# Performance work log

Measured on AMD Instinct MI355X. Metric: run time of the kernel, lower is better.

The kernel has to match this reference:

```python
import jax, jax.numpy as jnp
import numpy as np

L, H, V, T, E = 12, 12, 50257, 1024, 768
DH = E // H
EPS = 1e-5


def _ln(x, g, b):
    mu = jnp.mean(x, axis=-1, keepdims=True)
    var = jnp.mean(jnp.square(x - mu), axis=-1, keepdims=True)
    return g * (x - mu) * jax.lax.rsqrt(var + EPS) + b


def _gelu(x):
    # tanh-approx gelu as in the source
    return 0.5 * x * (1.0 + jnp.tanh(jnp.sqrt(2.0 / jnp.pi) * (x + 0.044715 * jnp.power(x, 3))))


def setup_inputs() -> dict:
    key = jax.random.key(0)
    ks = jax.random.split(key, 12)
    s = 0.02
    return {
        "x": jax.random.randint(ks[0], (8, T), 0, V),
        "tok_emb": jax.random.normal(ks[1], (V, E), jnp.float32) * s,
        "pos_emb": jax.random.normal(ks[2], (T, E), jnp.float32) * s,
        "ln1_g": jnp.ones((L, E), jnp.float32),
        "ln1_b": jnp.zeros((L, E), jnp.float32),
        "Wqkv": jax.random.normal(ks[3], (L, E, 3 * E), jnp.float32) * s,
        "bqkv": jnp.zeros((L, 3 * E), jnp.float32),
        "Wo": jax.random.normal(ks[4], (L, E, E), jnp.float32) * s,
        "bo": jnp.zeros((L, E), jnp.float32),
        "ln2_g": jnp.ones((L, E), jnp.float32),
        "ln2_b": jnp.zeros((L, E), jnp.float32),
        "W1": jax.random.normal(ks[5], (L, E, 4 * E), jnp.float32) * s,
        "b1": jnp.zeros((L, 4 * E), jnp.float32),
        "W2": jax.random.normal(ks[6], (L, 4 * E, E), jnp.float32) * s,
        "b2": jnp.zeros((L, E), jnp.float32),
        "lnf_g": jnp.ones((E,), jnp.float32),
        "lnf_b": jnp.zeros((E,), jnp.float32),
    }


def _gpt2(x, tok_emb, pos_emb, ln1_g, ln1_b, Wqkv, bqkv, Wo, bo,
          ln2_g, ln2_b, W1, b1, W2, b2, lnf_g, lnf_b):
    B, S = x.shape
    h = tok_emb[x] + pos_emb[:S][None, :, :]  # [B,S,E]
    mask = (jnp.arange(S)[:, None] >= jnp.arange(S)[None, :]).astype(jnp.float32)  # [S,S]
    mask = mask[None, None]  # [1,1,S,S]
    scale = jax.lax.rsqrt(jnp.float32(DH))
    for l in range(L):
        a = _ln(h, ln1_g[l], ln1_b[l])
        qkv = jnp.einsum('bse,ef->bsf', a, Wqkv[l]) + bqkv[l]
        q, k, v = jnp.split(qkv, 3, axis=-1)
        q = q.reshape(B, S, H, DH).transpose(0, 2, 1, 3)
        k = k.reshape(B, S, H, DH).transpose(0, 2, 1, 3)
        v = v.reshape(B, S, H, DH).transpose(0, 2, 1, 3)
        w = jnp.einsum('bhqd,bhkd->bhqk', q, k) * scale
        w = w * mask - 1e10 * (1.0 - mask)
        w = jax.nn.softmax(w, axis=-1)
        ctx = jnp.einsum('bhqk,bhkd->bhqd', w, v)
        ctx = ctx.transpose(0, 2, 1, 3).reshape(B, S, E)
        h = h + jnp.einsum('bse,ef->bsf', ctx, Wo[l]) + bo[l]
        a2 = _ln(h, ln2_g[l], ln2_b[l])
        ff = _gelu(jnp.einsum('bse,ef->bsf', a2, W1[l]) + b1[l])
        h = h + jnp.einsum('bsf,fe->bse', ff, W2[l]) + b2[l]
    h = _ln(h, lnf_g, lnf_b)
    last = h[:, -1, :]  # [B,E]
    return jnp.matmul(last, tok_emb.T)  # [B,V]


def reference(x, tok_emb, pos_emb, ln1_g, ln1_b, Wqkv, bqkv, Wo, bo,
              ln2_g, ln2_b, W1, b1, W2, b2, lnf_g, lnf_b):
    return _gpt2(x, tok_emb, pos_emb, ln1_g, ln1_b, Wqkv, bqkv, Wo, bo,
                 ln2_g, ln2_b, W1, b1, W2, b2, lnf_g, lnf_b)
```

## Files before the change

### kernel.cpp

```cpp
#include <hip/hip_runtime.h>
#include <math.h>

#define LNUM 12
#define HNUM 12
#define EMB 768
#define TSEQ 1024
#define BBATCH 8
#define VOCAB 50257
#define NTOK (BBATCH*TSEQ)

typedef unsigned short u16;
typedef __bf16 bf16_8 __attribute__((ext_vector_type(8)));
typedef float f32x4 __attribute__((ext_vector_type(4)));

__device__ __forceinline__ u16 f2bf(float f){
  unsigned u = __float_as_uint(f);
  u += 0x7fffu + ((u >> 16) & 1u);
  return (u16)(u >> 16);
}
__device__ __forceinline__ float wred(float v){
  #pragma unroll
  for (int m = 32; m; m >>= 1) v += __shfl_xor(v, m, 64);
  return v;
}

#define GLOAD_LDS16(g, l) \
  __builtin_amdgcn_global_load_lds((const __attribute__((address_space(1))) void*)(g), \
                                   (__attribute__((address_space(3))) void*)(l), 16, 0, 0)

__global__ __launch_bounds__(256) void tcvt_kernel(const float* __restrict__ src,
                                                   u16* __restrict__ dst, int K, int N){
  __shared__ float tile[32][33];
  size_t off = (size_t)blockIdx.z * K * N;
  const float* s = src + off;
  u16* d = dst + off;
  int n0 = blockIdx.x * 32, k0 = blockIdx.y * 32;
  int tx = threadIdx.x & 31, ty = threadIdx.x >> 5;
  #pragma unroll
  for (int i = 0; i < 4; i++)
    tile[ty + i*8][tx] = s[(size_t)(k0 + ty + i*8) * N + n0 + tx];
  __syncthreads();
  #pragma unroll
  for (int i = 0; i < 4; i++){
    int n = ty + i*8;
    d[(size_t)(n0 + n) * K + k0 + tx] = f2bf(tile[tx][n]);
  }
}

__global__ __launch_bounds__(256) void embed_kernel(const int* __restrict__ x,
    const float* __restrict__ tok, const float* __restrict__ pos, float* __restrict__ h){
  int row = blockIdx.x;
  int t = row & (TSEQ - 1);
  int id = x[row];
  const float* te = tok + (size_t)id * EMB;
  const float* pe = pos + (size_t)t * EMB;
  float* hr = h + (size_t)row * EMB;
  for (int i = threadIdx.x; i < EMB; i += 256) hr[i] = te[i] + pe[i];
}

template<int OBF, int LAST>
__global__ __launch_bounds__(256) void ln_kernel(const float* __restrict__ x,
    const float* __restrict__ g, const float* __restrict__ b, void* __restrict__ out){
  int orow, row;
  if (LAST){ orow = blockIdx.x; row = blockIdx.x * TSEQ + (TSEQ - 1); }
  else     { orow = row = blockIdx.x; }
  const float* xr = x + (size_t)row * EMB;
  int tid = threadIdx.x;
  int wave = tid >> 6, lane = tid & 63;
  float v[3];
  float s = 0.f;
  #pragma unroll
  for (int i = 0; i < 3; i++){ v[i] = xr[tid + i*256]; s += v[i]; }
  __shared__ float red[4];
  s = wred(s);
  if (lane == 0) red[wave] = s;
  __syncthreads();
  float mu = (red[0] + red[1] + red[2] + red[3]) * (1.f / EMB);
  float ss = 0.f;
  #pragma unroll
  for (int i = 0; i < 3; i++){ float d = v[i] - mu; ss += d * d; }
  __syncthreads();
  ss = wred(ss);
  if (lane == 0) red[wave] = ss;
  __syncthreads();
  float var = (red[0] + red[1] + red[2] + red[3]) * (1.f / EMB);
  float rs = rsqrtf(var + 1e-5f);
  #pragma unroll
  for (int i = 0; i < 3; i++){
    int e = tid + i*256;
    float o = g[e] * (v[i] - mu) * rs + b[e];
    if (OBF) ((u16*)out)[(size_t)orow * EMB + e] = f2bf(o);
    else     ((float*)out)[(size_t)orow * EMB + e] = o;
  }
}

template<int EPI>
__global__ __launch_bounds__(256) void gemm_bt(const u16* __restrict__ A,
    const u16* __restrict__ Bt, const float* __restrict__ bias,
    const float* __restrict__ resid, void* __restrict__ outp, int K, int N){
  __shared__ __align__(16) u16 lA[128*32];
  __shared__ __align__(16) u16 lB[128*32];
  const int tid = threadIdx.x;
  const int wave = tid >> 6, lane = tid & 63;
  const int bm = blockIdx.y, bn = blockIdx.x;
  const int wm = wave >> 1, wn = wave & 1;

  const u16* ga = A  + (size_t)(bm*128 + wave*32 + (lane >> 2)) * K + (lane & 3) * 8;
  const u16* gb = Bt + (size_t)(bn*128 + wave*32 + (lane >> 2)) * K + (lane & 3) * 8;
  u16* la = lA + wave * 32 * 32;
  u16* lb = lB + wave * 32 * 32;

  f32x4 acc[4][4];
  #pragma unroll
  for (int i = 0; i < 4; i++)
    #pragma unroll
    for (int j = 0; j < 4; j++){ f32x4 z = {0.f,0.f,0.f,0.f}; acc[i][j] = z; }

  const bf16_8* pa = (const bf16_8*)(lA + ((wm*64) + (lane & 15)) * 32 + (lane >> 4) * 8);
  const bf16_8* pb = (const bf16_8*)(lB + ((wn*64) + (lane & 15)) * 32 + (lane >> 4) * 8);

  for (int k0 = 0; k0 < K; k0 += 32){
    GLOAD_LDS16(ga,                 la);
    GLOAD_LDS16(ga + (size_t)16*K,  la + 16*32);
    GLOAD_LDS16(gb,                 lb);
    GLOAD_LDS16(gb + (size_t)16*K,  lb + 16*32);
    ga += 32; gb += 32;
    __syncthreads();
    bf16_8 af[4], bfv[4];
    #pragma unroll
    for (int i = 0; i < 4; i++){ af[i] = pa[i*64]; bfv[i] = pb[i*64]; }
    #pragma unroll
    for (int mi = 0; mi < 4; mi++)
      #pragma unroll
      for (int ni = 0; ni < 4; ni++)
        acc[mi][ni] = __builtin_amdgcn_mfma_f32_16x16x32_bf16(af[mi], bfv[ni], acc[mi][ni], 0, 0, 0);
    __syncthreads();
  }

  const int colb = bn*128 + wn*64;
  const int rowb = bm*128 + wm*64;
  #pragma unroll
  for (int ni = 0; ni < 4; ni++){
    int col = colb + ni*16 + (lane & 15);
    float bv = bias[col];
    #pragma unroll
    for (int mi = 0; mi < 4; mi++){
      #pragma unroll
      for (int j = 0; j < 4; j++){
        int row = rowb + mi*16 + (lane >> 4) * 4 + j;
        float v = acc[mi][ni][j] + bv;
        if (EPI == 1) v += resid[(size_t)row * N + col];
        if (EPI == 2){
          float y = 0.7978845608028654f * (v + 0.044715f * v * v * v);
          float e = __expf(fminf(2.f * y, 80.f));
          v = v * e / (e + 1.f);
        }
        if (EPI == 3 && col < 768) v *= 0.125f;
        if (EPI == 2 || EPI == 3) ((u16*)outp)[(size_t)row * N + col] = f2bf(v);
        else                      ((float*)outp)[(size_t)row * N + col] = v;
      }
    }
  }
}

__global__ __launch_bounds__(256) void vtrans_kernel(const u16* __restrict__ qkvb,
                                                     u16* __restrict__ vt){
  int wave = threadIdx.x >> 6, lane = threadIdx.x & 63;
  int bh = blockIdx.y, b = bh / HNUM, h = bh - b * HNUM;
  int t0 = blockIdx.x * 16 + wave * 4;
  const u16* src = qkvb + (size_t)b * TSEQ * 2304 + 1536 + h * 64 + lane;
  unsigned long long w = 0;
  #pragma unroll
  for (int i = 0; i < 4; i++)
    w |= (unsigned long long)src[(size_t)(t0 + i) * 2304] << (16 * i);
  *(unsigned long long*)(vt + ((size_t)bh * 64 + lane) * TSEQ + t0) = w;
}

__global__ __launch_bounds__(256) void attn_mfma(const u16* __restrict__ qkvb,
                                                 const u16* __restrict__ vt,
                                                 u16* __restrict__ ctx){
  __shared__ u16 plds[4][32][40];
  const int wave = threadIdx.x >> 6, lane = threadIdx.x & 63;
  const int g = lane >> 4, q15 = lane & 15;
  const int bh = blockIdx.y, b = bh / HNUM, h = bh - b * HNUM;
  const int q0 = blockIdx.x * 128 + wave * 32;
  const u16* qk  = qkvb + (size_t)b * TSEQ * 2304 + h * 64;
  const u16* vtb = vt + (size_t)bh * 64 * TSEQ;

  bf16_8 qfr[2][2];
  #pragma unroll
  for (int qf = 0; qf < 2; qf++)
    #pragma unroll
    for (int kc = 0; kc < 2; kc++)
      qfr[qf][kc] = *(const bf16_8*)(qk + (size_t)(q0 + qf*16 + q15) * 2304 + kc*32 + g*8);

  f32x4 oacc[2][4];
  #pragma unroll
  for (int i = 0; i < 2; i++)
    #pragma unroll
    for (int j = 0; j < 4; j++){ f32x4 z = {0.f,0.f,0.f,0.f}; oacc[i][j] = z; }
  float mx[2] = {-1e30f, -1e30f}, lsum[2] = {0.f, 0.f};

  for (int kb = 0; kb <= q0; kb += 32){
    bf16_8 kfr[2][2];
    #pragma unroll
    for (int kf = 0; kf < 2; kf++)
      #pragma unroll
      for (int kc = 0; kc < 2; kc++)
        kfr[kf][kc] = *(const bf16_8*)(qk + (size_t)(kb + kf*16 + q15) * 2304 + 768 + kc*32 + g*8);

    f32x4 s[2][2];
    #pragma unroll
    for (int kf = 0; kf < 2; kf++)
      #pragma unroll
      for (int qf = 0; qf < 2; qf++){
        f32x4 z = {0.f,0.f,0.f,0.f};
        #pragma unroll
        for (int kc = 0; kc < 2; kc++)
          z = __builtin_amdgcn_mfma_f32_16x16x32_bf16(kfr[kf][kc], qfr[qf][kc], z, 0, 0, 0);
        s[kf][qf] = z;
      }

    if (kb == q0){
      #pragma unroll
      for (int kf = 0; kf < 2; kf++)
        #pragma unroll
        for (int qf = 0; qf < 2; qf++)
          #pragma unroll
          for (int j = 0; j < 4; j++)
            if (kf*16 + g*4 + j > qf*16 + q15) s[kf][qf][j] = -1e30f;
    }

    bf16_8 vb[4];
    #pragma unroll
    for (int dc = 0; dc < 4; dc++)
      vb[dc] = *(const bf16_8*)(vtb + (size_t)(dc*16 + q15) * TSEQ + kb + g*8);

    #pragma unroll
    for (int qf = 0; qf < 2; qf++){
      float sm = -1e30f;
      #pragma unroll
      for (int kf = 0; kf < 2; kf++)
        #pragma unroll
        for (int j = 0; j < 4; j++) sm = fmaxf(sm, s[kf][qf][j]);
      sm = fmaxf(sm, __shfl_xor(sm, 16, 64));
      sm = fmaxf(sm, __shfl_xor(sm, 32, 64));
      float mn = fmaxf(mx[qf], sm);
      float c = __expf(mx[qf] - mn);
      mx[qf] = mn;
      float ps = 0.f;
      unsigned long long pw[2];
      #pragma unroll
      for (int kf = 0; kf < 2; kf++){
        unsigned long long w = 0;
        #pragma unroll
        for (int j = 0; j < 4; j++){
          float p = __expf(s[kf][qf][j] - mn);
          ps += p;
          w |= (unsigned long long)f2bf(p) << (16 * j);
        }
        pw[kf] = w;
      }
      ps += __shfl_xor(ps, 16, 64);
      ps += __shfl_xor(ps, 32, 64);
      lsum[qf] = lsum[qf] * c + ps;
      *(unsigned long long*)&plds[wave][qf*16 + q15][g*4]      = pw[0];
      *(unsigned long long*)&plds[wave][qf*16 + q15][16 + g*4] = pw[1];
      #pragma unroll
      for (int j = 0; j < 4; j++){
        float cr = __shfl(c, g*4 + j, 64);
        #pragma unroll
        for (int dc = 0; dc < 4; dc++) oacc[qf][dc][j] *= cr;
      }
    }

    asm volatile("s_waitcnt lgkmcnt(0)" ::: "memory");
    __builtin_amdgcn_sched_barrier(0);

    bf16_8 pa[2];
    pa[0] = *(const bf16_8*)&plds[wave][q15][g*8];
    pa[1] = *(const bf16_8*)&plds[wave][16 + q15][g*8];
    #pragma unroll
    for (int qf = 0; qf < 2; qf++)
      #pragma unroll
      for (int dc = 0; dc < 4; dc++)
        oacc[qf][dc] = __builtin_amdgcn_mfma_f32_16x16x32_bf16(pa[qf], vb[dc], oacc[qf][dc], 0, 0, 0);
  }

  u16* cb = ctx + ((size_t)(b * TSEQ + q0)) * EMB + h * 64;
  #pragma unroll
  for (int qf = 0; qf < 2; qf++){
    float inv = 1.f / lsum[qf];
    #pragma unroll
    for (int j = 0; j < 4; j++){
      float ir = __shfl(inv, g*4 + j, 64);
      int row = qf*16 + g*4 + j;
      #pragma unroll
      for (int dc = 0; dc < 4; dc++)
        cb[(size_t)row * EMB + dc*16 + q15] = f2bf(oacc[qf][dc][j] * ir);
    }
  }
}

__global__ __launch_bounds__(256) void logits_kernel(const float* __restrict__ last,
    const float* __restrict__ tok, float* __restrict__ out){
  __shared__ float ls[BBATCH * EMB];
  for (int i = threadIdx.x; i < BBATCH * EMB; i += 256) ls[i] = last[i];
  __syncthreads();
  int wave = threadIdx.x >> 6, lane = threadIdx.x & 63;
  int v = blockIdx.x * 4 + wave;
  if (v >= VOCAB) return;
  const float* tp = tok + (size_t)v * EMB;
  float acc[BBATCH];
  #pragma unroll
  for (int b = 0; b < BBATCH; b++) acc[b] = 0.f;
  #pragma unroll
  for (int i = 0; i < EMB/64; i++){
    float tv = tp[i*64 + lane];
    #pragma unroll
    for (int b = 0; b < BBATCH; b++) acc[b] += tv * ls[b*EMB + i*64 + lane];
  }
  #pragma unroll
  for (int b = 0; b < BBATCH; b++){
    float r = wred(acc[b]);
    if (lane == 0) out[(size_t)b * VOCAB + v] = r;
  }
}

extern "C" void kernel_launch(void* const* d_in, const int* in_sizes, int n_in,
                              void* d_out, int out_size, void* d_ws, size_t ws_size,
                              hipStream_t stream){
  const int*   x    = (const int*)  d_in[0];
  const float* tok  = (const float*)d_in[1];
  const float* pos  = (const float*)d_in[2];
  const float* ln1g = (const float*)d_in[3];
  const float* ln1b = (const float*)d_in[4];
  const float* Wqkv = (const float*)d_in[5];
  const float* bqkv = (const float*)d_in[6];
  const float* Wo   = (const float*)d_in[7];
  const float* bo   = (const float*)d_in[8];
  const float* ln2g = (const float*)d_in[9];
  const float* ln2b = (const float*)d_in[10];
  const float* W1   = (const float*)d_in[11];
  const float* b1   = (const float*)d_in[12];
  const float* W2   = (const float*)d_in[13];
  const float* b2   = (const float*)d_in[14];
  const float* lnfg = (const float*)d_in[15];
  const float* lnfb = (const float*)d_in[16];

  char* p = (char*)d_ws;
  u16* wqkvT = (u16*)p;  p += (size_t)LNUM*2304*768*2;
  u16* woT   = (u16*)p;  p += (size_t)LNUM*768*768*2;
  u16* w1T   = (u16*)p;  p += (size_t)LNUM*3072*768*2;
  u16* w2T   = (u16*)p;  p += (size_t)LNUM*768*3072*2;
  float* h   = (float*)p; p += (size_t)NTOK*EMB*4;
  u16* abuf  = (u16*)p;  p += (size_t)NTOK*EMB*2;
  void* tmp  = (void*)p; p += (size_t)NTOK*2304*4;
  u16* vt    = (u16*)p;  p += (size_t)BBATCH*HNUM*64*TSEQ*2;
  float* lastb = (float*)p; p += (size_t)BBATCH*EMB*4;
  if (ws_size < (size_t)(p - (char*)d_ws)) return;

  tcvt_kernel<<<dim3(2304/32, 768/32, LNUM), 256, 0, stream>>>(Wqkv, wqkvT, 768, 2304);
  tcvt_kernel<<<dim3(768/32,  768/32, LNUM), 256, 0, stream>>>(Wo,   woT,   768, 768);
  tcvt_kernel<<<dim3(3072/32, 768/32, LNUM), 256, 0, stream>>>(W1,   w1T,   768, 3072);
  tcvt_kernel<<<dim3(768/32, 3072/32, LNUM), 256, 0, stream>>>(W2,   w2T,   3072, 768);
  embed_kernel<<<NTOK, 256, 0, stream>>>(x, tok, pos, h);

  u16* qkvb = (u16*)tmp;
  u16* ff   = (u16*)tmp;
  for (int l = 0; l < LNUM; l++){
    ln_kernel<1,0><<<NTOK, 256, 0, stream>>>(h, ln1g + l*EMB, ln1b + l*EMB, abuf);
    gemm_bt<3><<<dim3(2304/128, NTOK/128), 256, 0, stream>>>(
        abuf, wqkvT + (size_t)l*2304*768, bqkv + (size_t)l*2304, nullptr, qkvb, 768, 2304);
    vtrans_kernel<<<dim3(TSEQ/16, BBATCH*HNUM), 256, 0, stream>>>(qkvb, vt);
    attn_mfma<<<dim3(TSEQ/128, BBATCH*HNUM), 256, 0, stream>>>(qkvb, vt, abuf);
    gemm_bt<1><<<dim3(768/128, NTOK/128), 256, 0, stream>>>(
        abuf, woT + (size_t)l*768*768, bo + (size_t)l*768, h, h, 768, 768);
    ln_kernel<1,0><<<NTOK, 256, 0, stream>>>(h, ln2g + l*EMB, ln2b + l*EMB, abuf);
    gemm_bt<2><<<dim3(3072/128, NTOK/128), 256, 0, stream>>>(
        abuf, w1T + (size_t)l*3072*768, b1 + (size_t)l*3072, nullptr, ff, 768, 3072);
    gemm_bt<1><<<dim3(768/128, NTOK/128), 256, 0, stream>>>(
        ff, w2T + (size_t)l*768*3072, b2 + (size_t)l*768, h, h, 3072, 768);
  }
  ln_kernel<0,1><<<BBATCH, 256, 0, stream>>>(h, lnfg, lnfb, lastb);
  logits_kernel<<<(VOCAB + 3)/4, 256, 0, stream>>>(lastb, tok, (float*)d_out);
}
```

Baseline: 4.333 ms.

## Pipeline GEMMs with 4-slot LDS ring and enlarge attention query tiles

Replaces the single-buffered 128x128 GEMM with a 512-thread kernel using larger tiles (128 or 256 by 256) and a four-slot LDS ring. Global-to-LDS loads are issued three K-steps ahead, and there is one barrier per step. This is meant to hide memory latency and cut synchronisation. Attention now gives each wave 64 query rows, prefetches the next K/V block into registers, and schedules the longest causal blocks first to improve load balance. The cost is higher register and LDS pressure, which may limit occupancy.

```diff
diff --git a/kernel.cpp b/kernel.cpp
--- a/kernel.cpp
+++ b/kernel.cpp
@@ -27,6 +27,8 @@
 #define GLOAD_LDS16(g, l) \
   __builtin_amdgcn_global_load_lds((const __attribute__((address_space(1))) void*)(g), \
                                    (__attribute__((address_space(3))) void*)(l), 16, 0, 0)
+
+template<int N> struct WCst { static constexpr int val = N; };
 
 __global__ __launch_bounds__(256) void tcvt_kernel(const float* __restrict__ src,
                                                    u16* __restrict__ dst, int K, int N){
@@ -94,60 +96,92 @@
   }
 }
 
-template<int EPI>
-__global__ __launch_bounds__(256) void gemm_bt(const u16* __restrict__ A,
+template<int BM, int EPI>
+__global__ __launch_bounds__(512, 2) void gemm_ring(const u16* __restrict__ A,
     const u16* __restrict__ Bt, const float* __restrict__ bias,
     const float* __restrict__ resid, void* __restrict__ outp, int K, int N){
-  __shared__ __align__(16) u16 lA[128*32];
-  __shared__ __align__(16) u16 lB[128*32];
+  constexpr int LA = BM / 128;
+  constexpr int LOADS = LA + 2;
+  constexpr int SLOTE = (BM + 256) * 32;
+  constexpr int M_REP = BM / 32;
+  __shared__ __align__(16) u16 lds[4 * SLOTE];
   const int tid = threadIdx.x;
   const int wave = tid >> 6, lane = tid & 63;
+  const int q15 = lane & 15, ko = lane >> 4;
+  const int wm = wave >> 2, wn = wave & 3;
   const int bm = blockIdx.y, bn = blockIdx.x;
-  const int wm = wave >> 1, wn = wave & 1;
-
-  const u16* ga = A  + (size_t)(bm*128 + wave*32 + (lane >> 2)) * K + (lane & 3) * 8;
-  const u16* gb = Bt + (size_t)(bn*128 + wave*32 + (lane >> 2)) * K + (lane & 3) * 8;
-  u16* la = lA + wave * 32 * 32;
-  u16* lb = lB + wave * 32 * 32;
-
-  f32x4 acc[4][4];
-  #pragma unroll
-  for (int i = 0; i < 4; i++)
+  const int NT = K >> 5;
+
+  const u16* gA0 = A  + (size_t)(bm*BM  + (tid >> 2)) * K + (tid & 3) * 8;
+  const u16* gB0 = Bt + (size_t)(bn*256 + (tid >> 2)) * K + (tid & 3) * 8;
+  u16* ldsW = lds + (tid >> 6) * 512;
+
+#define STAGE(tt) do { \
+    int _t = (tt); \
+    const u16* _sa = gA0 + (size_t)_t * 32; \
+    const u16* _sb = gB0 + (size_t)_t * 32; \
+    u16* _ls = ldsW + (_t & 3) * SLOTE; \
+    _Pragma("unroll") \
+    for (int _i = 0; _i < LA; _i++) \
+      GLOAD_LDS16(_sa + (size_t)_i * 128 * K, _ls + _i * 4096); \
+    _Pragma("unroll") \
+    for (int _i = 0; _i < 2; _i++) \
+      GLOAD_LDS16(_sb + (size_t)_i * 128 * K, _ls + BM*32 + _i * 4096); \
+  } while (0)
+
+  f32x4 acc[M_REP][4];
+  #pragma unroll
+  for (int i = 0; i < M_REP; i++)
     #pragma unroll
     for (int j = 0; j < 4; j++){ f32x4 z = {0.f,0.f,0.f,0.f}; acc[i][j] = z; }
 
-  const bf16_8* pa = (const bf16_8*)(lA + ((wm*64) + (lane & 15)) * 32 + (lane >> 4) * 8);
-  const bf16_8* pb = (const bf16_8*)(lB + ((wn*64) + (lane & 15)) * 32 + (lane >> 4) * 8);
-
-  for (int k0 = 0; k0 < K; k0 += 32){
-    GLOAD_LDS16(ga,                 la);
-    GLOAD_LDS16(ga + (size_t)16*K,  la + 16*32);
-    GLOAD_LDS16(gb,                 lb);
-    GLOAD_LDS16(gb + (size_t)16*K,  lb + 16*32);
-    ga += 32; gb += 32;
-    __syncthreads();
-    bf16_8 af[4], bfv[4];
-    #pragma unroll
-    for (int i = 0; i < 4; i++){ af[i] = pa[i*64]; bfv[i] = pb[i*64]; }
-    #pragma unroll
-    for (int mi = 0; mi < 4; mi++)
+  const int aoff = (wm*(BM/2) + q15) * 32 + ko * 8;
+  const int boff = BM*32 + (wn*64 + q15) * 32 + ko * 8;
+
+  auto tile = [&](int t, auto wc, bool dostage){
+    if (dostage) STAGE(t + 3);
+    const u16* sA = lds + (t & 3) * SLOTE;
+    bf16_8 af[M_REP], bfr[4];
+    #pragma unroll
+    for (int mi = 0; mi < M_REP; mi++) af[mi] = *(const bf16_8*)(sA + aoff + mi * 512);
+    #pragma unroll
+    for (int ni = 0; ni < 4; ni++)    bfr[ni] = *(const bf16_8*)(sA + boff + ni * 512);
+    __builtin_amdgcn_s_setprio(1);
+    #pragma unroll
+    for (int mi = 0; mi < M_REP; mi++)
       #pragma unroll
       for (int ni = 0; ni < 4; ni++)
-        acc[mi][ni] = __builtin_amdgcn_mfma_f32_16x16x32_bf16(af[mi], bfv[ni], acc[mi][ni], 0, 0, 0);
-    __syncthreads();
-  }
-
-  const int colb = bn*128 + wn*64;
-  const int rowb = bm*128 + wm*64;
+        acc[mi][ni] = __builtin_amdgcn_mfma_f32_16x16x32_bf16(af[mi], bfr[ni], acc[mi][ni], 0, 0, 0);
+    __builtin_amdgcn_s_setprio(0);
+    asm volatile("s_waitcnt vmcnt(%0)" :: "n"(decltype(wc)::val) : "memory");
+    __builtin_amdgcn_sched_barrier(0);
+    __builtin_amdgcn_s_barrier();
+    __builtin_amdgcn_sched_barrier(0);
+  };
+
+  STAGE(0); STAGE(1); STAGE(2);
+  asm volatile("s_waitcnt vmcnt(%0)" :: "n"(2 * LOADS) : "memory");
+  __builtin_amdgcn_sched_barrier(0);
+  __builtin_amdgcn_s_barrier();
+  __builtin_amdgcn_sched_barrier(0);
+
+  for (int t = 0; t < NT - 3; ++t) tile(t, WCst<2 * LOADS>{}, true);
+  tile(NT - 3, WCst<LOADS>{}, false);
+  tile(NT - 2, WCst<0>{}, false);
+  tile(NT - 1, WCst<0>{}, false);
+#undef STAGE
+
+  const int colb = bn*256 + wn*64;
+  const int rowb = bm*BM + wm*(BM/2);
   #pragma unroll
   for (int ni = 0; ni < 4; ni++){
-    int col = colb + ni*16 + (lane & 15);
+    int col = colb + ni*16 + q15;
     float bv = bias[col];
     #pragma unroll
-    for (int mi = 0; mi < 4; mi++){
+    for (int mi = 0; mi < M_REP; mi++){
       #pragma unroll
       for (int j = 0; j < 4; j++){
-        int row = rowb + mi*16 + (lane >> 4) * 4 + j;
+        int row = rowb + mi*16 + ko*4 + j;
         float v = acc[mi][ni][j] + bv;
         if (EPI == 1) v += resid[(size_t)row * N + col];
         if (EPI == 2){
@@ -176,68 +210,73 @@
   *(unsigned long long*)(vt + ((size_t)bh * 64 + lane) * TSEQ + t0) = w;
 }
 
-__global__ __launch_bounds__(256) void attn_mfma(const u16* __restrict__ qkvb,
-                                                 const u16* __restrict__ vt,
-                                                 u16* __restrict__ ctx){
-  __shared__ u16 plds[4][32][40];
+__global__ __launch_bounds__(256, 2) void attn_mfma(const u16* __restrict__ qkvb,
+                                                    const u16* __restrict__ vt,
+                                                    u16* __restrict__ ctx){
+  __shared__ u16 plds[4][64][40];
   const int wave = threadIdx.x >> 6, lane = threadIdx.x & 63;
   const int g = lane >> 4, q15 = lane & 15;
   const int bh = blockIdx.y, b = bh / HNUM, h = bh - b * HNUM;
-  const int q0 = blockIdx.x * 128 + wave * 32;
+  const int q0 = ((int)gridDim.x - 1 - (int)blockIdx.x) * 256 + wave * 64;
   const u16* qk  = qkvb + (size_t)b * TSEQ * 2304 + h * 64;
   const u16* vtb = vt + (size_t)bh * 64 * TSEQ;
 
-  bf16_8 qfr[2][2];
-  #pragma unroll
-  for (int qf = 0; qf < 2; qf++)
+#define LOADKV(kb_, kd, vd) do { \
+    _Pragma("unroll") \
+    for (int _kf = 0; _kf < 2; _kf++) \
+      _Pragma("unroll") \
+      for (int _kc = 0; _kc < 2; _kc++) \
+        kd[_kf][_kc] = *(const bf16_8*)(qk + (size_t)((kb_) + _kf*16 + q15) * 2304 + 768 + _kc*32 + g*8); \
+    _Pragma("unroll") \
+    for (int _dc = 0; _dc < 4; _dc++) \
+      vd[_dc] = *(const bf16_8*)(vtb + (size_t)(_dc*16 + q15) * TSEQ + (kb_) + g*8); \
+  } while (0)
+
+  bf16_8 qfr[4][2];
+  #pragma unroll
+  for (int qf = 0; qf < 4; qf++)
     #pragma unroll
     for (int kc = 0; kc < 2; kc++)
       qfr[qf][kc] = *(const bf16_8*)(qk + (size_t)(q0 + qf*16 + q15) * 2304 + kc*32 + g*8);
 
-  f32x4 oacc[2][4];
-  #pragma unroll
-  for (int i = 0; i < 2; i++)
+  f32x4 oacc[4][4];
+  #pragma unroll
+  for (int i = 0; i < 4; i++)
     #pragma unroll
     for (int j = 0; j < 4; j++){ f32x4 z = {0.f,0.f,0.f,0.f}; oacc[i][j] = z; }
-  float mx[2] = {-1e30f, -1e30f}, lsum[2] = {0.f, 0.f};
-
-  for (int kb = 0; kb <= q0; kb += 32){
-    bf16_8 kfr[2][2];
+  float mx[4] = {-1e30f,-1e30f,-1e30f,-1e30f}, lsum[4] = {0.f,0.f,0.f,0.f};
+
+  const int kbmax = q0 + 32;
+  bf16_8 kcur[2][2], vcur[4];
+  LOADKV(0, kcur, vcur);
+
+  for (int kb = 0; kb <= kbmax; kb += 32){
+    bf16_8 knxt[2][2], vnxt[4];
+    if (kb < kbmax) LOADKV(kb + 32, knxt, vnxt);
+
+    f32x4 s[2][4];
     #pragma unroll
     for (int kf = 0; kf < 2; kf++)
       #pragma unroll
-      for (int kc = 0; kc < 2; kc++)
-        kfr[kf][kc] = *(const bf16_8*)(qk + (size_t)(kb + kf*16 + q15) * 2304 + 768 + kc*32 + g*8);
-
-    f32x4 s[2][2];
-    #pragma unroll
-    for (int kf = 0; kf < 2; kf++)
-      #pragma unroll
-      for (int qf = 0; qf < 2; qf++){
+      for (int qf = 0; qf < 4; qf++){
         f32x4 z = {0.f,0.f,0.f,0.f};
-        #pragma unroll
-        for (int kc = 0; kc < 2; kc++)
-          z = __builtin_amdgcn_mfma_f32_16x16x32_bf16(kfr[kf][kc], qfr[qf][kc], z, 0, 0, 0);
+        z = __builtin_amdgcn_mfma_f32_16x16x32_bf16(kcur[kf][0], qfr[qf][0], z, 0, 0, 0);
+        z = __builtin_amdgcn_mfma_f32_16x16x32_bf16(kcur[kf][1], qfr[qf][1], z, 0, 0, 0);
         s[kf][qf] = z;
       }
 
-    if (kb == q0){
+    if (kb + 31 > q0){
       #pragma unroll
       for (int kf = 0; kf < 2; kf++)
         #pragma unroll
-        for (int qf = 0; qf < 2; qf++)
+        for (int qf = 0; qf < 4; qf++)
           #pragma unroll
           for (int j = 0; j < 4; j++)
-            if (kf*16 + g*4 + j > qf*16 + q15) s[kf][qf][j] = -1e30f;
+            if (kb + kf*16 + g*4 + j > q0 + qf*16 + q15) s[kf][qf][j] = -1e30f;
     }
 
-    bf16_8 vb[4];
-    #pragma unroll
-    for (int dc = 0; dc < 4; dc++)
-      vb[dc] = *(const bf16_8*)(vtb + (size_t)(dc*16 + q15) * TSEQ + kb + g*8);
-
-    #pragma unroll
-    for (int qf = 0; qf < 2; qf++){
+    #pragma unroll
+    for (int qf = 0; qf < 4; qf++){
       float sm = -1e30f;
       #pragma unroll
       for (int kf = 0; kf < 2; kf++)
@@ -277,19 +316,30 @@
     asm volatile("s_waitcnt lgkmcnt(0)" ::: "memory");
     __builtin_amdgcn_sched_barrier(0);
 
-    bf16_8 pa[2];
-    pa[0] = *(const bf16_8*)&plds[wave][q15][g*8];
-    pa[1] = *(const bf16_8*)&plds[wave][16 + q15][g*8];
-    #pragma unroll
-    for (int qf = 0; qf < 2; qf++)
+    bf16_8 pa[4];
+    #pragma unroll
+    for (int qf = 0; qf < 4; qf++)
+      pa[qf] = *(const bf16_8*)&plds[wave][qf*16 + q15][g*8];
+    #pragma unroll
+    for (int qf = 0; qf < 4; qf++)
       #pragma unroll
       for (int dc = 0; dc < 4; dc++)
-        oacc[qf][dc] = __builtin_amdgcn_mfma_f32_16x16x32_bf16(pa[qf], vb[dc], oacc[qf][dc], 0, 0, 0);
-  }
+        oacc[qf][dc] = __builtin_amdgcn_mfma_f32_16x16x32_bf16(pa[qf], vcur[dc], oacc[qf][dc], 0, 0, 0);
+
+    if (kb < kbmax){
+      #pragma unroll
+      for (int kf = 0; kf < 2; kf++)
+        #pragma unroll
+        for (int kc = 0; kc < 2; kc++) kcur[kf][kc] = knxt[kf][kc];
+      #pragma unroll
+      for (int dc = 0; dc < 4; dc++) vcur[dc] = vnxt[dc];
+    }
+  }
+#undef LOADKV
 
   u16* cb = ctx + ((size_t)(b * TSEQ + q0)) * EMB + h * 64;
   #pragma unroll
-  for (int qf = 0; qf < 2; qf++){
+  for (int qf = 0; qf < 4; qf++){
     float inv = 1.f / lsum[qf];
     #pragma unroll
     for (int j = 0; j < 4; j++){
@@ -370,16 +420,16 @@
   u16* ff   = (u16*)tmp;
   for (int l = 0; l < LNUM; l++){
     ln_kernel<1,0><<<NTOK, 256, 0, stream>>>(h, ln1g + l*EMB, ln1b + l*EMB, abuf);
-    gemm_bt<3><<<dim3(2304/128, NTOK/128), 256, 0, stream>>>(
+    gemm_ring<128,3><<<dim3(2304/256, NTOK/128), 512, 0, stream>>>(
         abuf, wqkvT + (size_t)l*2304*768, bqkv + (size_t)l*2304, nullptr, qkvb, 768, 2304);
     vtrans_kernel<<<dim3(TSEQ/16, BBATCH*HNUM), 256, 0, stream>>>(qkvb, vt);
-    attn_mfma<<<dim3(TSEQ/128, BBATCH*HNUM), 256, 0, stream>>>(qkvb, vt, abuf);
-    gemm_bt<1><<<dim3(768/128, NTOK/128), 256, 0, stream>>>(
+    attn_mfma<<<dim3(TSEQ/256, BBATCH*HNUM), 256, 0, stream>>>(qkvb, vt, abuf);
+    gemm_ring<128,1><<<dim3(768/256, NTOK/128), 512, 0, stream>>>(
         abuf, woT + (size_t)l*768*768, bo + (size_t)l*768, h, h, 768, 768);
     ln_kernel<1,0><<<NTOK, 256, 0, stream>>>(h, ln2g + l*EMB, ln2b + l*EMB, abuf);
-    gemm_bt<2><<<dim3(3072/128, NTOK/128), 256, 0, stream>>>(
+    gemm_ring<256,2><<<dim3(3072/256, NTOK/256), 512, 0, stream>>>(
         abuf, w1T + (size_t)l*3072*768, b1 + (size_t)l*3072, nullptr, ff, 768, 3072);
-    gemm_bt<1><<<dim3(768/128, NTOK/128), 256, 0, stream>>>(
+    gemm_ring<128,1><<<dim3(768/256, NTOK/128), 512, 0, stream>>>(
         ff, w2T + (size_t)l*768*3072, b2 + (size_t)l*768, h, h, 3072, 768);
   }
   ln_kernel<0,1><<<BBATCH, 256, 0, stream>>>(h, lnfg, lnfb, lastb);
```

After: 3.934 ms. 9.2% less time.
